# Kernel tuning notes

Measured on AMD Instinct MI355X. Metric: run time of the kernel, lower is better.

Reference implementation:

```python
import jax, jax.numpy as jnp
import numpy as np

B, T, H, V, ADIM, AMAX = 16, 1024, 512, 32000, 512, 10


def setup_inputs() -> dict:
    key = jax.random.key(0)
    ks = jax.random.split(key, 24)
    def n(k, shape, s=0.05):
        return jax.random.normal(k, shape, jnp.float32) * s
    return {
        "instruction": jax.random.randint(ks[0], (B, T), 0, V, dtype=jnp.int32),
        "emb": n(ks[1], (V, H)),
        "wih_f": n(ks[2], (4 * H, H)), "whh_f": n(ks[3], (4 * H, H)),
        "bih_f": n(ks[4], (4 * H,)), "bhh_f": n(ks[5], (4 * H,)),
        "wih_b": n(ks[6], (4 * H, H)), "whh_b": n(ks[7], (4 * H, H)),
        "bih_b": n(ks[8], (4 * H,)), "bhh_b": n(ks[9], (4 * H,)),
        "wg": n(ks[10], (2 * H, 2 * H)), "bg": n(ks[11], (2 * H,)),
        "ws1": n(ks[12], (H, 2 * H)), "bs1": n(ks[13], (H,)),
        "ws2": n(ks[14], (1, H)), "bs2": n(ks[15], (1,)),
        "wd1": n(ks[16], (H, 2 * H)), "bd1": n(ks[17], (H,)),
        "wd2": n(ks[18], (ADIM, H)), "bd2": n(ks[19], (ADIM,)),
        "max_actions": AMAX,
    }


def _lstm(x, wih, whh, bias):
    # x: [B, T, H] -> outputs [B, T, H]; PyTorch gate order i, f, g, o
    h0 = jnp.zeros((x.shape[0], whh.shape[1]), x.dtype)
    def step(carry, xt):
        h, c = carry
        g = xt @ wih.T + h @ whh.T + bias
        i, f, gg, o = jnp.split(g, 4, axis=-1)
        c = jax.nn.sigmoid(f) * c + jax.nn.sigmoid(i) * jnp.tanh(gg)
        h = jax.nn.sigmoid(o) * jnp.tanh(c)
        return (h, c), h
    _, hs = jax.lax.scan(step, (h0, h0), jnp.swapaxes(x, 0, 1))
    return jnp.swapaxes(hs, 0, 1)


def reference(instruction, emb, wih_f, whh_f, bih_f, bhh_f, wih_b, whh_b, bih_b, bhh_b,
              wg, bg, ws1, bs1, ws2, bs2, wd1, bd1, wd2, bd2, max_actions):
    x = emb[instruction]                                   # [B, T, H]
    fwd = _lstm(x, wih_f, whh_f, bih_f + bhh_f)            # [B, T, H]
    bwd = _lstm(x[:, ::-1], wih_b, whh_b, bih_b + bhh_b)[:, ::-1]
    enc = jnp.concatenate([fwd, bwd], axis=-1)             # [B, T, 2H]
    # sequence_lengths=None: h_n[0]=fwd last step, h_n[1]=bwd at t=0
    pooled = jnp.concatenate([fwd[:, -1], bwd[:, 0]], axis=-1)
    gctx = pooled @ wg.T + bg                               # [B, 2H]
    sh = jax.nn.relu(enc @ ws1.T + bs1)
    seg_probs = jax.nn.sigmoid((sh @ ws2.T + bs2)[..., 0])  # [B, T]
    mask = seg_probs > 0.5
    count = mask.sum(axis=-1)
    # first max_actions True positions per row (stable sort keeps time order)
    order = jnp.argsort(jnp.logical_not(mask), axis=1, stable=True)[:, :max_actions]
    gathered = jnp.take_along_axis(enc, order[..., None], axis=1)  # [B, A, 2H]
    slots = jnp.arange(max_actions)
    valid = slots[None, :] < jnp.minimum(count, max_actions)[:, None]
    empty = ((count == 0)[:, None]) & (slots[None, :] == 0)  # fallback: decode global ctx
    dec_in = jnp.where(valid[..., None], gathered, 0.0)
    dec_in = jnp.where(empty[..., None], gctx[:, None, :], dec_in)
    dh = jax.nn.relu(dec_in @ wd1.T + bd1)
    actions = (dh @ wd2.T + bd2) * (valid | empty)[..., None].astype(dec_in.dtype)
    return actions, seg_probs
```

## Files before the change

kernel.cpp:

```cpp
#include <hip/hip_runtime.h>
#include <math.h>

#define T   1024
#define NB  16
#define HD  512

#define OFF_BAR  0
#define OFF_HH   256
#define OFF_SH   (OFF_HH + 16777216)
#define OFF_SEGP (OFF_SH + 8388608)
#define OFF_GCTX (OFF_SEGP + 16384)
#define OFF_SEL  (OFF_GCTX + 16384)

typedef unsigned long long u64;

__device__ __forceinline__ float sigmoidf_(float x){ return 1.0f/(1.0f + __expf(-x)); }
__device__ __forceinline__ float tanhf_(float x){ return 1.0f - 2.0f/(1.0f + __expf(2.0f*x)); }

__global__ __launch_bounds__(512, 1)
void lstm_kernel(const int* __restrict__ instr, const float* __restrict__ emb,
                 const float* __restrict__ wih_f, const float* __restrict__ whh_f,
                 const float* __restrict__ bih_f, const float* __restrict__ bhh_f,
                 const float* __restrict__ wih_b, const float* __restrict__ whh_b,
                 const float* __restrict__ bih_b, const float* __restrict__ bhh_b,
                 float* __restrict__ ws)
{
    float* h_hist = ws + OFF_HH;
    int* flags = (int*)ws;

    const int wg     = blockIdx.x;
    const int dir    = wg & 1;
    const int bgrp   = (wg >> 1) & 3;
    const int uslice = wg >> 3;
    const int U      = uslice * 16;
    const int b0     = bgrp * 4;

    int* barf = flags + (dir*4 + bgrp)*32;

    const float* wih = dir ? wih_b : wih_f;
    const float* whh = dir ? whh_b : whh_f;
    const float* bih = dir ? bih_b : bih_f;
    const float* bhh = dir ? bhh_b : bhh_f;

    const int tid  = threadIdx.x;
    const int wid  = tid >> 6;
    const int lane = tid & 63;
    const int rg   = wid;

    float wi[64], wh[64];
#pragma unroll
    for (int ri = 0; ri < 8; ++ri){
        int rgl = rg*8 + ri;
        int gate = rgl >> 4, ul = rgl & 15;
        size_t row = (size_t)(gate*HD + U + ul) * HD + lane*8;
        float4 a0 = *(const float4*)(wih + row);
        float4 a1 = *(const float4*)(wih + row + 4);
        float4 b0v = *(const float4*)(whh + row);
        float4 b1v = *(const float4*)(whh + row + 4);
        wi[ri*8+0]=a0.x; wi[ri*8+1]=a0.y; wi[ri*8+2]=a0.z; wi[ri*8+3]=a0.w;
        wi[ri*8+4]=a1.x; wi[ri*8+5]=a1.y; wi[ri*8+6]=a1.z; wi[ri*8+7]=a1.w;
        wh[ri*8+0]=b0v.x; wh[ri*8+1]=b0v.y; wh[ri*8+2]=b0v.z; wh[ri*8+3]=b0v.w;
        wh[ri*8+4]=b1v.x; wh[ri*8+5]=b1v.y; wh[ri*8+6]=b1v.z; wh[ri*8+7]=b1v.w;
    }

    float bI, bF, bG, bO, cst = 0.0f;
    {
        int u = tid & 15;
        bI = bih[0*HD + U + u] + bhh[0*HD + U + u];
        bF = bih[1*HD + U + u] + bhh[1*HD + U + u];
        bG = bih[2*HD + U + u] + bhh[2*HD + U + u];
        bO = bih[3*HD + U + u] + bhh[3*HD + U + u];
    }

    __shared__ float gbuf[256];

    const int jown = ((lane&1)<<4)|((lane&2)<<2)|(lane&4)|((lane&8)>>2)|((lane&16)>>4);
    const int own_bi  = jown >> 3;
    const int own_rgl = rg*8 + (jown & 7);
    const int gslot   = (own_rgl >> 4)*64 + own_bi*16 + (own_rgl & 15);

    for (int s = 0; s < T; ++s){
        const int tp = dir ? (T-1-s) : s;

        float a[32];
#pragma unroll
        for (int j = 0; j < 32; ++j) a[j] = 0.0f;

#pragma unroll
        for (int bi = 0; bi < 4; ++bi){
            int b = b0 + bi;
            int idx = instr[b*T + tp];
            const float* px = emb + (size_t)idx*HD + lane*8;
            float4 x0 = *(const float4*)px;
            float4 x1 = *(const float4*)(px + 4);
            float xs[8] = {x0.x,x0.y,x0.z,x0.w,x1.x,x1.y,x1.z,x1.w};
#pragma unroll
            for (int kk = 0; kk < 8; ++kk){
                float xv = xs[kk];
#pragma unroll
                for (int ri = 0; ri < 8; ++ri)
                    a[bi*8+ri] = fmaf(xv, wi[ri*8+kk], a[bi*8+ri]);
            }
        }

        if (s > 0){
            if (wid == 0){
                for (;;){
                    int v = __hip_atomic_load(barf + (lane & 31), __ATOMIC_RELAXED, __HIP_MEMORY_SCOPE_AGENT);
                    if (__all(v >= s)) break;
                    __builtin_amdgcn_s_sleep(1);
                }
            }
            __syncthreads();

            const int tprev = dir ? (T - s) : (s - 1);
            const float* hbase = h_hist + (size_t)(dir*T + tprev)*NB*HD;
#pragma unroll
            for (int bi = 0; bi < 4; ++bi){
                int b = b0 + bi;
                const float* ph = hbase + (size_t)b*HD + lane*8;
                float4 h0 = *(const float4*)ph;
                float4 h1 = *(const float4*)(ph + 4);
                float hs[8] = {h0.x,h0.y,h0.z,h0.w,h1.x,h1.y,h1.z,h1.w};
#pragma unroll
                for (int kk = 0; kk < 8; ++kk){
                    float hv = hs[kk];
#pragma unroll
                    for (int ri = 0; ri < 8; ++ri)
                        a[bi*8+ri] = fmaf(hv, wh[ri*8+kk], a[bi*8+ri]);
                }
            }
        }

#pragma unroll
        for (int m = 0; m < 5; ++m){
            const int half = 16 >> m;
            const bool up = (lane >> m) & 1;
#pragma unroll
            for (int j = 0; j < 16; ++j){
                if (j < half){
                    float lo = a[j], hi = a[j+half];
                    float rlo = __shfl_xor(lo, 1<<m, 64);
                    float rhi = __shfl_xor(hi, 1<<m, 64);
                    a[j] = up ? (hi + rhi) : (lo + rlo);
                }
            }
        }
        a[0] += __shfl_xor(a[0], 32, 64);

        if ((lane & 32) == 0) gbuf[gslot] = a[0];
        __syncthreads();

        if (tid < 64){
            float iv = sigmoidf_(gbuf[      tid] + bI);
            float fv = sigmoidf_(gbuf[ 64 + tid] + bF);
            float gv = tanhf_  (gbuf[128 + tid] + bG);
            float ov = sigmoidf_(gbuf[192 + tid] + bO);
            cst = fv*cst + iv*gv;
            float hv = ov * tanhf_(cst);
            int b = b0 + (tid >> 4), u = tid & 15;
            __hip_atomic_store(&h_hist[((size_t)(dir*T + tp)*NB + b)*HD + U + u], hv,
                               __ATOMIC_RELAXED, __HIP_MEMORY_SCOPE_AGENT);
        }
        asm volatile("s_waitcnt vmcnt(0)" ::: "memory");
        __builtin_amdgcn_sched_barrier(0);
        if (tid == 0)
            __hip_atomic_store(barf + uslice, s + 1, __ATOMIC_RELAXED, __HIP_MEMORY_SCOPE_AGENT);
    }
}

__global__ __launch_bounds__(256, 2)
void seg_gemm(const float* __restrict__ ws_, const float* __restrict__ ws1,
              const float* __restrict__ bs1)
{
    const float* h_hist = ws_ + OFF_HH;
    float* SH = (float*)(ws_ + OFF_SH);
    __shared__ float As[64][17];
    __shared__ float Bs[64][17];
    const int m0 = blockIdx.x * 64;
    const int n0 = blockIdx.y * 64;
    const int tid = threadIdx.x;
    const int r  = tid >> 2;
    const int kq = (tid & 3) * 4;
    const int ty = tid >> 4, tx = tid & 15;
    const int bI = m0 >> 10;
    const int t0 = m0 & 1023;

    float acc[4][4];
#pragma unroll
    for (int i=0;i<4;i++)
#pragma unroll
        for (int j=0;j<4;j++) acc[i][j]=0.0f;

    for (int kb = 0; kb < 1024; kb += 16){
        int kk = kb + kq;
        const float* ap = (kk < 512)
            ? h_hist + ((size_t)(t0 + r)*NB + bI)*HD + kk
            : h_hist + ((size_t)(T + t0 + r)*NB + bI)*HD + (kk - 512);
        float4 av = *(const float4*)ap;
        As[r][kq+0]=av.x; As[r][kq+1]=av.y; As[r][kq+2]=av.z; As[r][kq+3]=av.w;
        float4 bv = *(const float4*)(ws1 + (size_t)(n0 + r)*1024 + kk);
        Bs[r][kq+0]=bv.x; Bs[r][kq+1]=bv.y; Bs[r][kq+2]=bv.z; Bs[r][kq+3]=bv.w;
        __syncthreads();
#pragma unroll
        for (int k2 = 0; k2 < 16; ++k2){
            float av_[4], bv_[4];
#pragma unroll
            for (int i=0;i<4;i++) av_[i] = As[ty*4+i][k2];
#pragma unroll
            for (int j=0;j<4;j++) bv_[j] = Bs[tx*4+j][k2];
#pragma unroll
            for (int i=0;i<4;i++)
#pragma unroll
                for (int j=0;j<4;j++) acc[i][j] = fmaf(av_[i], bv_[j], acc[i][j]);
        }
        __syncthreads();
    }
#pragma unroll
    for (int i=0;i<4;i++){
        int m = m0 + ty*4 + i;
#pragma unroll
        for (int j=0;j<4;j++){
            int n = n0 + tx*4 + j;
            SH[(size_t)m*512 + n] = fmaxf(acc[i][j] + bs1[n], 0.0f);
        }
    }
}

__global__ void seg_score(const float* __restrict__ ws_, const float* __restrict__ ws2,
                          const float* __restrict__ bs2, float* __restrict__ dout)
{
    const float* SH = ws_ + OFF_SH;
    float* segp = (float*)(ws_ + OFF_SEGP);
    int row  = blockIdx.x*4 + (threadIdx.x >> 6);
    int lane = threadIdx.x & 63;
    const float* p = SH + (size_t)row*512 + lane*8;
    const float* q = ws2 + lane*8;
    float4 a0=*(const float4*)p, a1=*(const float4*)(p+4);
    float4 b0=*(const float4*)q, b1=*(const float4*)(q+4);
    float ssum = a0.x*b0.x + a0.y*b0.y + a0.z*b0.z + a0.w*b0.w
               + a1.x*b1.x + a1.y*b1.y + a1.z*b1.z + a1.w*b1.w;
#pragma unroll
    for (int m=1;m<64;m<<=1) ssum += __shfl_xor(ssum, m, 64);
    if (lane == 0){
        float z = ssum + bs2[0];
        float pr = 1.0f/(1.0f + __expf(-z));
        segp[row] = pr;
        dout[81920 + row] = pr;
    }
}

__global__ void select_gctx(float* __restrict__ ws_, const float* __restrict__ wgm,
                            const float* __restrict__ bgv)
{
    const float* h_hist = ws_ + OFF_HH;
    const float* segp   = ws_ + OFF_SEGP;
    float* gctx = ws_ + OFF_GCTX;
    int* sel = (int*)(ws_ + OFF_SEL);
    int b = blockIdx.x, tid = threadIdx.x;
    __shared__ unsigned char flag[1024];
    __shared__ float pool[1024];
    for (int j = tid; j < 1024; j += 256){
        flag[j] = segp[b*1024 + j] > 0.5f ? 1 : 0;
        pool[j] = (j < 512) ? h_hist[((size_t)1023*NB + b)*HD + j]
                            : h_hist[((size_t)T*NB + b)*HD + (j - 512)];
    }
    __syncthreads();
    if (tid == 0){
        int c = 0;
        int tmp[10];
        for (int j = 0; j < 10; ++j) tmp[j] = 0;
        for (int t = 0; t < 1024; ++t){
            if (flag[t]){ if (c < 10) tmp[c] = t; c++; }
        }
        for (int j = 0; j < 10; ++j) sel[b*12 + j] = tmp[j];
        sel[b*12 + 10] = c;
        sel[b*12 + 11] = 0;
    }
    __syncthreads();
    for (int n = tid; n < 1024; n += 256){
        float acc = bgv[n];
        const float* wr = wgm + (size_t)n*1024;
        for (int k = 0; k < 1024; k += 4){
            acc += wr[k]*pool[k] + wr[k+1]*pool[k+1] + wr[k+2]*pool[k+2] + wr[k+3]*pool[k+3];
        }
        gctx[b*1024 + n] = acc;
    }
}

__global__ void decode(const float* __restrict__ ws_, const float* __restrict__ wd1,
                       const float* __restrict__ bd1, const float* __restrict__ wd2,
                       const float* __restrict__ bd2, float* __restrict__ dout)
{
    const float* h_hist = ws_ + OFF_HH;
    const float* gctx   = ws_ + OFF_GCTX;
    const int* sel = (const int*)(ws_ + OFF_SEL);
    int blk = blockIdx.x;
    int b = blk / 10, slot = blk % 10;
    int tid = threadIdx.x;
    int count = sel[b*12 + 10];
    int nval = count < 10 ? count : 10;
    bool empty = (count == 0);
    float* outp = dout + (size_t)(b*10 + slot)*512;
    if (slot >= nval && !(empty && slot == 0)){
        for (int n = tid; n < 512; n += 256) outp[n] = 0.0f;
        return;
    }
    __shared__ float row[1024];
    __shared__ float dh[512];
    if (empty){
        for (int j = tid; j < 1024; j += 256) row[j] = gctx[b*1024 + j];
    } else {
        int t = sel[b*12 + slot];
        for (int j = tid; j < 1024; j += 256)
            row[j] = (j < 512) ? h_hist[((size_t)t*NB + b)*HD + j]
                               : h_hist[((size_t)(T + t)*NB + b)*HD + (j-512)];
    }
    __syncthreads();
    for (int d = tid; d < 512; d += 256){
        float acc = bd1[d];
        const float* wr = wd1 + (size_t)d*1024;
        for (int k = 0; k < 1024; ++k) acc += wr[k]*row[k];
        dh[d] = fmaxf(acc, 0.0f);
    }
    __syncthreads();
    for (int n = tid; n < 512; n += 256){
        float acc = bd2[n];
        const float* wr = wd2 + (size_t)n*512;
        for (int k = 0; k < 512; ++k) acc += wr[k]*dh[k];
        outp[n] = acc;
    }
}

extern "C" void kernel_launch(void* const* d_in, const int* in_sizes, int n_in,
                              void* d_out, int out_size, void* d_ws, size_t ws_size,
                              hipStream_t stream)
{
    const int*   instr = (const int*)d_in[0];
    const float* emb   = (const float*)d_in[1];
    const float* wih_f = (const float*)d_in[2];
    const float* whh_f = (const float*)d_in[3];
    const float* bih_f = (const float*)d_in[4];
    const float* bhh_f = (const float*)d_in[5];
    const float* wih_b = (const float*)d_in[6];
    const float* whh_b = (const float*)d_in[7];
    const float* bih_b = (const float*)d_in[8];
    const float* bhh_b = (const float*)d_in[9];
    const float* wg_   = (const float*)d_in[10];
    const float* bg_   = (const float*)d_in[11];
    const float* ws1   = (const float*)d_in[12];
    const float* bs1   = (const float*)d_in[13];
    const float* ws2   = (const float*)d_in[14];
    const float* bs2   = (const float*)d_in[15];
    const float* wd1   = (const float*)d_in[16];
    const float* bd1   = (const float*)d_in[17];
    const float* wd2   = (const float*)d_in[18];
    const float* bd2   = (const float*)d_in[19];
    float* out = (float*)d_out;
    float* ws  = (float*)d_ws;

    hipMemsetAsync(d_ws, 0, 1024, stream);

    hipLaunchKernelGGL(lstm_kernel, dim3(256), dim3(512), 0, stream,
                       instr, emb, wih_f, whh_f, bih_f, bhh_f,
                       wih_b, whh_b, bih_b, bhh_b, ws);
    hipLaunchKernelGGL(seg_gemm, dim3(256, 8), dim3(256), 0, stream, ws, ws1, bs1);
    hipLaunchKernelGGL(seg_score, dim3(4096), dim3(256), 0, stream, ws, ws2, bs2, out);
    hipLaunchKernelGGL(select_gctx, dim3(16), dim3(256), 0, stream, ws, wg_, bg_);
    hipLaunchKernelGGL(decode, dim3(160), dim3(256), 0, stream, ws, wd1, bd1, wd2, bd2, out);
}
```

Before: 4.465 ms.

## Pipeline LSTM steps per batch element with sentinel-based h readiness

Each timestep is split into four sub-steps, one per batch element, each with its own reduction, gate computation and barrier counter. This lets different waves wait on different barrier targets, so one batch element's h can be consumed while others are still being produced. The h history buffer is pre-filled with 0xFF as a NaN sentinel so readers can spin on the data itself rather than a flag. The next embedding row is also prefetched one sub-step ahead. The cost is an extra 64MB memset, four __syncthreads pairs per step instead of two, and spin-loop overhead.

```diff
diff --git a/kernel.cpp b/kernel.cpp
--- a/kernel.cpp
+++ b/kernel.cpp
@@ -45,12 +45,11 @@
     const int tid  = threadIdx.x;
     const int wid  = tid >> 6;
     const int lane = tid & 63;
-    const int rg   = wid;
 
     float wi[64], wh[64];
 #pragma unroll
     for (int ri = 0; ri < 8; ++ri){
-        int rgl = rg*8 + ri;
+        int rgl = wid*8 + ri;
         int gate = rgl >> 4, ul = rgl & 15;
         size_t row = (size_t)(gate*HD + U + ul) * HD + lane*8;
         float4 a0 = *(const float4*)(wih + row);
@@ -65,107 +64,150 @@
 
     float bI, bF, bG, bO, cst = 0.0f;
     {
-        int u = tid & 15;
+        int u = lane & 15;
         bI = bih[0*HD + U + u] + bhh[0*HD + U + u];
         bF = bih[1*HD + U + u] + bhh[1*HD + U + u];
         bG = bih[2*HD + U + u] + bhh[2*HD + U + u];
         bO = bih[3*HD + U + u] + bhh[3*HD + U + u];
     }
 
-    __shared__ float gbuf[256];
-
-    const int jown = ((lane&1)<<4)|((lane&2)<<2)|(lane&4)|((lane&8)>>2)|((lane&16)>>4);
-    const int own_bi  = jown >> 3;
-    const int own_rgl = rg*8 + (jown & 7);
-    const int gslot   = (own_rgl >> 4)*64 + own_bi*16 + (own_rgl & 15);
+    __shared__ float gbuf[64];
+
+    const int jown3 = ((lane&1)<<2) | (lane&2) | ((lane&4)>>2);
+
+    float4 xq[2][2];
+    {
+        int t0 = dir ? (T-1) : 0;
+        int idx = instr[(b0+0)*T + t0];
+        const float* px = emb + (size_t)idx*HD + lane*8;
+        xq[0][0] = *(const float4*)px;
+        xq[0][1] = *(const float4*)(px + 4);
+    }
 
     for (int s = 0; s < T; ++s){
-        const int tp = dir ? (T-1-s) : s;
-
-        float a[32];
-#pragma unroll
-        for (int j = 0; j < 32; ++j) a[j] = 0.0f;
+        const int tp  = dir ? (T-1-s) : s;
+        const int tpn = dir ? (T-2-s) : (s+1);
+        const int tprev = dir ? (tp+1) : (tp-1);
 
 #pragma unroll
         for (int bi = 0; bi < 4; ++bi){
-            int b = b0 + bi;
-            int idx = instr[b*T + tp];
-            const float* px = emb + (size_t)idx*HD + lane*8;
-            float4 x0 = *(const float4*)px;
-            float4 x1 = *(const float4*)(px + 4);
-            float xs[8] = {x0.x,x0.y,x0.z,x0.w,x1.x,x1.y,x1.z,x1.w};
-#pragma unroll
-            for (int kk = 0; kk < 8; ++kk){
-                float xv = xs[kk];
-#pragma unroll
-                for (int ri = 0; ri < 8; ++ri)
-                    a[bi*8+ri] = fmaf(xv, wi[ri*8+kk], a[bi*8+ri]);
-            }
-        }
-
-        if (s > 0){
-            if (wid == 0){
+            const int cur = bi & 1, nxt = (bi+1) & 1;
+            const int bN = (bi+1) & 3;
+            const int tN = (bi < 3) ? tp : tpn;
+            const bool haveN = (bi < 3) || (s+1 < T);
+
+            if (s > 0 && wid == 4+bi){
+                const int tgt = s*4 + bi - 3;
                 for (;;){
-                    int v = __hip_atomic_load(barf + (lane & 31), __ATOMIC_RELAXED, __HIP_MEMORY_SCOPE_AGENT);
-                    if (__all(v >= s)) break;
+                    int v = (lane < 32)
+                        ? __hip_atomic_load(barf + lane, __ATOMIC_RELAXED, __HIP_MEMORY_SCOPE_AGENT)
+                        : 0x7fffffff;
+                    if (__all(v >= tgt)) break;
                     __builtin_amdgcn_s_sleep(1);
                 }
             }
             __syncthreads();
 
-            const int tprev = dir ? (T - s) : (s - 1);
-            const float* hbase = h_hist + (size_t)(dir*T + tprev)*NB*HD;
-#pragma unroll
-            for (int bi = 0; bi < 4; ++bi){
-                int b = b0 + bi;
-                const float* ph = hbase + (size_t)b*HD + lane*8;
-                float4 h0 = *(const float4*)ph;
-                float4 h1 = *(const float4*)(ph + 4);
-                float hs[8] = {h0.x,h0.y,h0.z,h0.w,h1.x,h1.y,h1.z,h1.w};
+            float4 hq0, hq1;
+            const float* hb = h_hist + ((size_t)(dir*T + tprev)*NB + b0 + bi)*HD + lane*8;
+            if (s > 0){
+                hq0 = *(const float4*)hb;
+                hq1 = *(const float4*)(hb + 4);
+            }
+
+            if (haveN){
+                int idx = instr[(b0+bN)*T + tN];
+                const float* px = emb + (size_t)idx*HD + lane*8;
+                xq[nxt][0] = *(const float4*)px;
+                xq[nxt][1] = *(const float4*)(px + 4);
+            }
+
+            float a[8];
+#pragma unroll
+            for (int j = 0; j < 8; ++j) a[j] = 0.0f;
+            {
+                float xs[8] = {xq[cur][0].x,xq[cur][0].y,xq[cur][0].z,xq[cur][0].w,
+                               xq[cur][1].x,xq[cur][1].y,xq[cur][1].z,xq[cur][1].w};
+#pragma unroll
+                for (int kk = 0; kk < 8; ++kk){
+                    float xv = xs[kk];
+#pragma unroll
+                    for (int ri = 0; ri < 8; ++ri)
+                        a[ri] = fmaf(xv, wi[ri*8+kk], a[ri]);
+                }
+            }
+
+            if (s > 0){
+                unsigned ok = 1u;
+                ok &= (__float_as_uint(hq0.x)!=0xFFFFFFFFu); ok &= (__float_as_uint(hq0.y)!=0xFFFFFFFFu);
+                ok &= (__float_as_uint(hq0.z)!=0xFFFFFFFFu); ok &= (__float_as_uint(hq0.w)!=0xFFFFFFFFu);
+                ok &= (__float_as_uint(hq1.x)!=0xFFFFFFFFu); ok &= (__float_as_uint(hq1.y)!=0xFFFFFFFFu);
+                ok &= (__float_as_uint(hq1.z)!=0xFFFFFFFFu); ok &= (__float_as_uint(hq1.w)!=0xFFFFFFFFu);
+                while (!__all(ok != 0u)){
+                    const u64* p = (const u64*)hb;
+                    u64 q0 = __hip_atomic_load(p+0, __ATOMIC_RELAXED, __HIP_MEMORY_SCOPE_AGENT);
+                    u64 q1 = __hip_atomic_load(p+1, __ATOMIC_RELAXED, __HIP_MEMORY_SCOPE_AGENT);
+                    u64 q2 = __hip_atomic_load(p+2, __ATOMIC_RELAXED, __HIP_MEMORY_SCOPE_AGENT);
+                    u64 q3 = __hip_atomic_load(p+3, __ATOMIC_RELAXED, __HIP_MEMORY_SCOPE_AGENT);
+                    float2 f0 = __builtin_bit_cast(float2, q0);
+                    float2 f1 = __builtin_bit_cast(float2, q1);
+                    float2 f2 = __builtin_bit_cast(float2, q2);
+                    float2 f3 = __builtin_bit_cast(float2, q3);
+                    hq0 = make_float4(f0.x,f0.y,f1.x,f1.y);
+                    hq1 = make_float4(f2.x,f2.y,f3.x,f3.y);
+                    ok = 1u;
+                    ok &= (__float_as_uint(hq0.x)!=0xFFFFFFFFu); ok &= (__float_as_uint(hq0.y)!=0xFFFFFFFFu);
+                    ok &= (__float_as_uint(hq0.z)!=0xFFFFFFFFu); ok &= (__float_as_uint(hq0.w)!=0xFFFFFFFFu);
+                    ok &= (__float_as_uint(hq1.x)!=0xFFFFFFFFu); ok &= (__float_as_uint(hq1.y)!=0xFFFFFFFFu);
+                    ok &= (__float_as_uint(hq1.z)!=0xFFFFFFFFu); ok &= (__float_as_uint(hq1.w)!=0xFFFFFFFFu);
+                }
+                float hs[8] = {hq0.x,hq0.y,hq0.z,hq0.w,hq1.x,hq1.y,hq1.z,hq1.w};
 #pragma unroll
                 for (int kk = 0; kk < 8; ++kk){
                     float hv = hs[kk];
 #pragma unroll
                     for (int ri = 0; ri < 8; ++ri)
-                        a[bi*8+ri] = fmaf(hv, wh[ri*8+kk], a[bi*8+ri]);
-                }
+                        a[ri] = fmaf(hv, wh[ri*8+kk], a[ri]);
+                }
+            }
+
+#pragma unroll
+            for (int m = 0; m < 3; ++m){
+                const int half = 4 >> m;
+                const bool up = (lane >> m) & 1;
+#pragma unroll
+                for (int j = 0; j < 4; ++j){
+                    if (j < half){
+                        float lo = a[j], hi = a[j+half];
+                        float rlo = __shfl_xor(lo, 1<<m, 64);
+                        float rhi = __shfl_xor(hi, 1<<m, 64);
+                        a[j] = up ? (hi + rhi) : (lo + rlo);
+                    }
+                }
+            }
+            a[0] += __shfl_xor(a[0], 8, 64);
+            a[0] += __shfl_xor(a[0], 16, 64);
+            a[0] += __shfl_xor(a[0], 32, 64);
+
+            if (lane < 8) gbuf[wid*8 + jown3] = a[0];
+            __syncthreads();
+
+            if (wid == bi){
+                if (lane < 16){
+                    float iv = sigmoidf_(gbuf[      lane] + bI);
+                    float fv = sigmoidf_(gbuf[ 16 + lane] + bF);
+                    float gv = tanhf_  (gbuf[ 32 + lane] + bG);
+                    float ov = sigmoidf_(gbuf[ 48 + lane] + bO);
+                    cst = fv*cst + iv*gv;
+                    float hv = ov * tanhf_(cst);
+                    __hip_atomic_store(&h_hist[((size_t)(dir*T + tp)*NB + b0 + bi)*HD + U + lane], hv,
+                                       __ATOMIC_RELAXED, __HIP_MEMORY_SCOPE_AGENT);
+                }
+                if (lane == 0)
+                    __hip_atomic_store(barf + uslice, s*4 + bi + 1,
+                                       __ATOMIC_RELAXED, __HIP_MEMORY_SCOPE_AGENT);
             }
         }
-
-#pragma unroll
-        for (int m = 0; m < 5; ++m){
-            const int half = 16 >> m;
-            const bool up = (lane >> m) & 1;
-#pragma unroll
-            for (int j = 0; j < 16; ++j){
-                if (j < half){
-                    float lo = a[j], hi = a[j+half];
-                    float rlo = __shfl_xor(lo, 1<<m, 64);
-                    float rhi = __shfl_xor(hi, 1<<m, 64);
-                    a[j] = up ? (hi + rhi) : (lo + rlo);
-                }
-            }
-        }
-        a[0] += __shfl_xor(a[0], 32, 64);
-
-        if ((lane & 32) == 0) gbuf[gslot] = a[0];
-        __syncthreads();
-
-        if (tid < 64){
-            float iv = sigmoidf_(gbuf[      tid] + bI);
-            float fv = sigmoidf_(gbuf[ 64 + tid] + bF);
-            float gv = tanhf_  (gbuf[128 + tid] + bG);
-            float ov = sigmoidf_(gbuf[192 + tid] + bO);
-            cst = fv*cst + iv*gv;
-            float hv = ov * tanhf_(cst);
-            int b = b0 + (tid >> 4), u = tid & 15;
-            __hip_atomic_store(&h_hist[((size_t)(dir*T + tp)*NB + b)*HD + U + u], hv,
-                               __ATOMIC_RELAXED, __HIP_MEMORY_SCOPE_AGENT);
-        }
-        asm volatile("s_waitcnt vmcnt(0)" ::: "memory");
-        __builtin_amdgcn_sched_barrier(0);
-        if (tid == 0)
-            __hip_atomic_store(barf + uslice, s + 1, __ATOMIC_RELAXED, __HIP_MEMORY_SCOPE_AGENT);
     }
 }
 
@@ -360,6 +402,7 @@
     float* ws  = (float*)d_ws;
 
     hipMemsetAsync(d_ws, 0, 1024, stream);
+    hipMemsetAsync((char*)d_ws + (size_t)OFF_HH*4, 0xFF, (size_t)16777216*4, stream);
 
     hipLaunchKernelGGL(lstm_kernel, dim3(256), dim3(512), 0, stream,
                        instr, emb, wih_f, whh_f, bih_f, bhh_f,
```

Result: slower. 9.388 ms (+110.3%).
